# Performance work log

Measured on AMD Instinct MI355X. Metric: run time of the kernel, lower is better.

Reference implementation:

```python
import jax, jax.numpy as jnp
import numpy as np

B, D, K, A, P = 4096, 512, 128, 32, 16  # batch, theta dim, mixture comps, alpha dim, hutchinson probes


def setup_inputs() -> dict:
    key = jax.random.key(0)
    k1, k2, k3, k4 = jax.random.split(key, 4)
    thetas = jax.random.normal(k1, (B, D), dtype=jnp.float32)
    alpha = jax.random.normal(k2, (K, A), dtype=jnp.float32)
    W = jax.random.normal(k3, (A, D), dtype=jnp.float32) / jnp.sqrt(jnp.float32(A))
    v_int = jax.random.randint(k4, (P, B, D), 0, 2, dtype=jnp.int32)  # -> Rademacher via 2v-1
    return {"thetas": thetas, "alpha": alpha, "W": W, "v_int": v_int,
            "N_dataset": 100000, "K_alpha_samples": K}


def _log_density(thetas, alpha, W, N_dataset, K_alpha):
    # Tempered Gaussian mixture: mu_k = alpha_k @ W;
    # logp_b = (N/(N+1)) * (logsumexp_k -0.5||theta_b - mu_k||^2 - log K)
    mu = alpha @ W                                        # [K, D]
    # ||t - mu||^2 expanded to avoid a [B,K,D] intermediate
    sq = (jnp.sum(thetas * thetas, -1, keepdims=True)
          - 2.0 * thetas @ mu.T
          + jnp.sum(mu * mu, -1)[None, :])                # [B, K]
    temper = jnp.float32(N_dataset) / (jnp.float32(N_dataset) + 1.0)
    return temper * (jax.nn.logsumexp(-0.5 * sq, axis=1) - jnp.log(jnp.float32(K_alpha)))


def reference(thetas, alpha, W, v_int, N_dataset, K_alpha_samples):
    v = (2 * v_int - 1).astype(thetas.dtype)              # [P, B, D] Rademacher

    def logp_sum(t):
        return jnp.sum(_log_density(t, alpha, W, N_dataset, K_alpha_samples))

    score = jax.grad(logp_sum)                            # gradiente wrt thetas
    g = score(thetas)                                     # [B, D]

    # Hutchinson trace of the per-sample Hessian via forward-over-reverse HVPs,
    # batched over probes (fuses the torch per-probe autograd.grad loop).
    def hvp(vi):
        return jax.jvp(score, (thetas,), (vi,))[1]        # [B, D]

    Hv = jax.vmap(hvp)(v)                                 # [P, B, D]
    traces = jnp.mean(jnp.sum(v * Hv, axis=-1), axis=0)   # [B]

    loss = 0.5 * jnp.sum(g * g, axis=-1) + traces         # [B]
    return jnp.mean(loss)
```

## Files before the change

### kernel.cpp

```cpp
#include <hip/hip_runtime.h>
#include <hip/hip_bf16.h>
#include <stdint.h>

#define Bsz 4096
#define Dn  512
#define Kn  128
#define Pn  16
#define An  32
#define TB  16

typedef __attribute__((ext_vector_type(4))) float  floatx4;
typedef __attribute__((ext_vector_type(8))) short  shortx8;

__device__ __forceinline__ unsigned short f2bf(float x) {
    union { float f; uint32_t u; } v; v.f = x;
    uint32_t u = v.u;
    uint32_t r = (u + 0x7FFFu + ((u >> 16) & 1u)) >> 16;
    return (unsigned short)r;
}

__global__ __launch_bounds__(256) void k_mu(const float* __restrict__ alpha,
                                            const float* __restrict__ W,
                                            float* __restrict__ mu_f,
                                            unsigned short* __restrict__ mu_bf,
                                            float* __restrict__ munorm) {
    __shared__ float al[An];
    __shared__ float red[4];
    int k = blockIdx.x, t = threadIdx.x;
    if (t < An) al[t] = alpha[k * An + t];
    __syncthreads();
    int d0 = t, d1 = t + 256;
    float a0 = 0.f, a1 = 0.f;
#pragma unroll
    for (int a = 0; a < An; ++a) {
        float av = al[a];
        a0 = fmaf(av, W[a * Dn + d0], a0);
        a1 = fmaf(av, W[a * Dn + d1], a1);
    }
    mu_f[k * Dn + d0] = a0;  mu_f[k * Dn + d1] = a1;
    mu_bf[k * Dn + d0] = f2bf(a0);  mu_bf[k * Dn + d1] = f2bf(a1);
    float nrm = a0 * a0 + a1 * a1;
#pragma unroll
    for (int msk = 1; msk < 64; msk <<= 1) nrm += __shfl_xor(nrm, msk);
    if ((t & 63) == 0) red[t >> 6] = nrm;
    __syncthreads();
    if (t == 0) munorm[k] = red[0] + red[1] + red[2] + red[3];
}

__global__ __launch_bounds__(256) void k_gram(const float* __restrict__ mu_f,
                                              unsigned short* __restrict__ G_bf) {
    __shared__ float mi[Dn];
    __shared__ float hsum[128];
    int i = blockIdx.x, t = threadIdx.x;
    mi[t] = mu_f[i * Dn + t];
    mi[t + 256] = mu_f[i * Dn + t + 256];
    __syncthreads();
    int j = t >> 1, h = t & 1;
    const float* rj = mu_f + (size_t)j * Dn + h * 256;
    const float* ri = mi + h * 256;
    float acc = 0.f;
#pragma unroll 8
    for (int d = 0; d < 256; ++d) acc = fmaf(ri[d], rj[d], acc);
    if (h) hsum[j] = acc;
    __syncthreads();
    if (!h) G_bf[i * Kn + j] = f2bf(acc + hsum[j]);
}

__global__ __launch_bounds__(512, 2) void k_main(
    const float* __restrict__ thetas,
    const int* __restrict__ v_int,
    const unsigned short* __restrict__ mu_bf,
    const float* __restrict__ munorm,
    const unsigned short* __restrict__ G_bf,
    const int* __restrict__ Np,
    float* __restrict__ out)
{
    __shared__ short vt[TB][520];
    __shared__ float S_l[TB][132];
    __shared__ float w_l[TB][132];
    __shared__ short wbf[TB][136];
    __shared__ float part[8][TB][2];
    __shared__ float thn[TB];
    __shared__ float SwS[TB];

    const int tid = threadIdx.x;
    const int lane = tid & 63;
    const int wv = tid >> 6;
    const int m = lane & 15;
    const int q = lane >> 4;

    const int tileb = blockIdx.x >> 1;
    const int phalf = blockIdx.x & 1;
    const int b0 = tileb * TB;
    const int p0 = phalf * 8;

    const float Nf = (float)(*Np);
    const float temper = Nf / (Nf + 1.0f);

    const int kcol = wv * 16 + m;
    shortx8 mufrag[16];
    {
        const unsigned short* mb = mu_bf + (size_t)kcol * Dn + q * 8;
#pragma unroll
        for (int dc = 0; dc < 16; ++dc)
            mufrag[dc] = *(const shortx8*)(mb + dc * 32);
    }
    shortx8 gfrag[4];
    {
        const unsigned short* gb = G_bf + (size_t)kcol * Kn + q * 8;
#pragma unroll
        for (int kc = 0; kc < 4; ++kc)
            gfrag[kc] = *(const shortx8*)(gb + kc * 32);
    }

    const int r = tid >> 5;
    const int c0 = (tid & 31) * 16;
    const size_t PB = (size_t)Bsz * Dn;
    const int* vrow = v_int + (size_t)(b0 + r) * Dn + c0;

    int4 buf[2][4];
    {
        const int4* g = (const int4*)(vrow + (size_t)p0 * PB);
#pragma unroll
        for (int j = 0; j < 4; ++j) buf[0][j] = g[j];
    }
    {
        const float4* tg = (const float4*)(thetas + (size_t)(b0 + r) * Dn + c0);
        float tn = 0.f;
#pragma unroll
        for (int j = 0; j < 4; ++j) {
            float4 f = tg[j];
            tn += f.x * f.x + f.y * f.y + f.z * f.z + f.w * f.w;
            short4 h;
            h.x = (short)f2bf(f.x); h.y = (short)f2bf(f.y);
            h.z = (short)f2bf(f.z); h.w = (short)f2bf(f.w);
            *(short4*)&vt[r][c0 + j * 4] = h;
        }
#pragma unroll
        for (int msk = 1; msk < 32; msk <<= 1) tn += __shfl_xor(tn, msk);
        if ((tid & 31) == 0) thn[r] = tn;
    }
    __syncthreads();

    {
        floatx4 acc = {0.f, 0.f, 0.f, 0.f};
#pragma unroll
        for (int dc = 0; dc < 16; ++dc) {
            shortx8 a = *(const shortx8*)&vt[m][dc * 32 + q * 8];
            acc = __builtin_amdgcn_mfma_f32_16x16x32_bf16(a, mufrag[dc], acc, 0, 0, 0);
        }
#pragma unroll
        for (int i = 0; i < 4; ++i) S_l[q * 4 + i][kcol] = acc[i];
    }
    __syncthreads();

    {
        const int b = tid >> 5, s = tid & 31;
        float l[4];
        float mx = -3.4e38f;
        float tnb = thn[b];
#pragma unroll
        for (int j = 0; j < 4; ++j) {
            int k = s + 32 * j;
            l[j] = -0.5f * (tnb - 2.f * S_l[b][k] + munorm[k]);
            mx = fmaxf(mx, l[j]);
        }
#pragma unroll
        for (int msk = 1; msk < 32; msk <<= 1) mx = fmaxf(mx, __shfl_xor(mx, msk));
        float se = 0.f, ses = 0.f;
        float e[4];
#pragma unroll
        for (int j = 0; j < 4; ++j) {
            int k = s + 32 * j;
            e[j] = __expf(l[j] - mx);
            se += e[j];
            ses += e[j] * S_l[b][k];
        }
#pragma unroll
        for (int msk = 1; msk < 32; msk <<= 1) { se += __shfl_xor(se, msk); ses += __shfl_xor(ses, msk); }
        float inv = 1.f / se;
#pragma unroll
        for (int j = 0; j < 4; ++j) {
            int k = s + 32 * j;
            float wvv = e[j] * inv;
            w_l[b][k] = wvv;
            wbf[b][k] = (short)f2bf(wvv);
        }
        if (s == 0) SwS[b] = ses * inv;
    }
    __syncthreads();

    float lossA = 0.f;
    {
        floatx4 acc = {0.f, 0.f, 0.f, 0.f};
#pragma unroll
        for (int kc = 0; kc < 4; ++kc) {
            shortx8 a = *(const shortx8*)&wbf[m][kc * 32 + q * 8];
            acc = __builtin_amdgcn_mfma_f32_16x16x32_bf16(a, gfrag[kc], acc, 0, 0, 0);
        }
        float sg[4];
#pragma unroll
        for (int i = 0; i < 4; ++i) sg[i] = w_l[q * 4 + i][kcol] * acc[i];
#pragma unroll
        for (int msk = 1; msk < 16; msk <<= 1) {
#pragma unroll
            for (int i = 0; i < 4; ++i) sg[i] += __shfl_xor(sg[i], msk);
        }
        if (m == 0) {
#pragma unroll
            for (int i = 0; i < 4; ++i) part[wv][q * 4 + i][0] = sg[i];
        }
    }
    __syncthreads();
    if (tid < TB) {
        float wGw = 0.f;
#pragma unroll
        for (int w8 = 0; w8 < 8; ++w8) wGw += part[w8][tid][0];
        if (phalf == 0)
            lossA = 0.5f * temper * temper * (wGw - 2.f * SwS[tid] + thn[tid])
                    - temper * (float)Dn;
    }

    float tracc = 0.f;
#pragma unroll
    for (int p = 0; p < 8; ++p) {
        if (p < 7) {
            const int4* g = (const int4*)(vrow + (size_t)(p0 + p + 1) * PB);
#pragma unroll
            for (int j = 0; j < 4; ++j) buf[(p + 1) & 1][j] = g[j];
        }
#pragma unroll
        for (int j = 0; j < 4; ++j) {
            int4 w4 = buf[p & 1][j];
            short4 h;
            h.x = (short)(0x3F80 | ((1 - w4.x) << 15));
            h.y = (short)(0x3F80 | ((1 - w4.y) << 15));
            h.z = (short)(0x3F80 | ((1 - w4.z) << 15));
            h.w = (short)(0x3F80 | ((1 - w4.w) << 15));
            *(short4*)&vt[r][c0 + j * 4] = h;
        }
        __syncthreads();
        floatx4 acc = {0.f, 0.f, 0.f, 0.f};
#pragma unroll
        for (int dc = 0; dc < 16; ++dc) {
            shortx8 a = *(const shortx8*)&vt[m][dc * 32 + q * 8];
            acc = __builtin_amdgcn_mfma_f32_16x16x32_bf16(a, mufrag[dc], acc, 0, 0, 0);
        }
        float s1[4], s2[4];
#pragma unroll
        for (int i = 0; i < 4; ++i) {
            float T = acc[i];
            float wt = w_l[q * 4 + i][kcol];
            s1[i] = wt * T * T;
            s2[i] = wt * T;
        }
#pragma unroll
        for (int msk = 1; msk < 16; msk <<= 1) {
#pragma unroll
            for (int i = 0; i < 4; ++i) {
                s1[i] += __shfl_xor(s1[i], msk);
                s2[i] += __shfl_xor(s2[i], msk);
            }
        }
        if (m == 0) {
#pragma unroll
            for (int i = 0; i < 4; ++i) {
                part[wv][q * 4 + i][0] = s1[i];
                part[wv][q * 4 + i][1] = s2[i];
            }
        }
        __syncthreads();
        if (tid < TB) {
            float S1 = 0.f, S2 = 0.f;
#pragma unroll
            for (int w8 = 0; w8 < 8; ++w8) { S1 += part[w8][tid][0]; S2 += part[w8][tid][1]; }
            tracc += S1 - S2 * S2;
        }
    }

    if (tid < TB) {
        float res = temper * tracc * (1.0f / (float)Pn) + lossA;
#pragma unroll
        for (int msk = 1; msk < 16; msk <<= 1) res += __shfl_xor(res, msk);
        if (tid == 0) atomicAdd(out, res * (1.0f / (float)Bsz));
    }
}

extern "C" void kernel_launch(void* const* d_in, const int* in_sizes, int n_in,
                              void* d_out, int out_size, void* d_ws, size_t ws_size,
                              hipStream_t stream) {
    const float* thetas = (const float*)d_in[0];
    const float* alpha  = (const float*)d_in[1];
    const float* W      = (const float*)d_in[2];
    const int*   v_int  = (const int*)d_in[3];
    const int*   Np     = (const int*)d_in[4];

    char* ws = (char*)d_ws;
    float*          mu_f   = (float*)ws;
    unsigned short* mu_bf  = (unsigned short*)(ws + 262144);
    float*          munorm = (float*)(ws + 262144 + 131072);
    unsigned short* G_bf   = (unsigned short*)(ws + 262144 + 131072 + 1024);

    float* out = (float*)d_out;
    hipMemsetAsync(out, 0, sizeof(float), stream);
    k_mu  <<<dim3(Kn),  dim3(256), 0, stream>>>(alpha, W, mu_f, mu_bf, munorm);
    k_gram<<<dim3(Kn),  dim3(256), 0, stream>>>(mu_f, G_bf);
    k_main<<<dim3(512), dim3(512), 0, stream>>>(thetas, v_int, mu_bf, munorm, G_bf, Np, out);
}
```

Measured before the change: 224.5 us.

## Double-buffer probe tiles, MFMA gram kernel, fold memset, raise occupancy

The probe loop now double-buffers both the LDS probe tile and the partial-sum array, so each iteration needs one barrier instead of two and the reduction of the previous probe overlaps the next MFMA. The gram matrix is computed with bf16 MFMA from mu_bf in 8 blocks, which also removes the fp32 mu buffer. The output memset is folded into k_mu, gfrag loading is deferred to cut register pressure, and launch bounds are raised to 4 blocks per CU. The larger LDS footprint may cap the occupancy actually reached, and bf16 precision in the gram matrix changes numerics slightly.

```diff
diff --git a/kernel.cpp b/kernel.cpp
--- a/kernel.cpp
+++ b/kernel.cpp
@@ -21,12 +21,13 @@
 
 __global__ __launch_bounds__(256) void k_mu(const float* __restrict__ alpha,
                                             const float* __restrict__ W,
-                                            float* __restrict__ mu_f,
                                             unsigned short* __restrict__ mu_bf,
-                                            float* __restrict__ munorm) {
+                                            float* __restrict__ munorm,
+                                            float* __restrict__ out) {
     __shared__ float al[An];
     __shared__ float red[4];
     int k = blockIdx.x, t = threadIdx.x;
+    if (k == 0 && t == 0) *out = 0.f;
     if (t < An) al[t] = alpha[k * An + t];
     __syncthreads();
     int d0 = t, d1 = t + 256;
@@ -37,7 +38,6 @@
         a0 = fmaf(av, W[a * Dn + d0], a0);
         a1 = fmaf(av, W[a * Dn + d1], a1);
     }
-    mu_f[k * Dn + d0] = a0;  mu_f[k * Dn + d1] = a1;
     mu_bf[k * Dn + d0] = f2bf(a0);  mu_bf[k * Dn + d1] = f2bf(a1);
     float nrm = a0 * a0 + a1 * a1;
 #pragma unroll
@@ -47,26 +47,40 @@
     if (t == 0) munorm[k] = red[0] + red[1] + red[2] + red[3];
 }
 
-__global__ __launch_bounds__(256) void k_gram(const float* __restrict__ mu_f,
+__global__ __launch_bounds__(512) void k_gram(const unsigned short* __restrict__ mu_bf,
                                               unsigned short* __restrict__ G_bf) {
-    __shared__ float mi[Dn];
-    __shared__ float hsum[128];
-    int i = blockIdx.x, t = threadIdx.x;
-    mi[t] = mu_f[i * Dn + t];
-    mi[t + 256] = mu_f[i * Dn + t + 256];
-    __syncthreads();
-    int j = t >> 1, h = t & 1;
-    const float* rj = mu_f + (size_t)j * Dn + h * 256;
-    const float* ri = mi + h * 256;
-    float acc = 0.f;
-#pragma unroll 8
-    for (int d = 0; d < 256; ++d) acc = fmaf(ri[d], rj[d], acc);
-    if (h) hsum[j] = acc;
-    __syncthreads();
-    if (!h) G_bf[i * Kn + j] = f2bf(acc + hsum[j]);
-}
-
-__global__ __launch_bounds__(512, 2) void k_main(
+    __shared__ short at[TB][520];
+    const int tid = threadIdx.x;
+    const int lane = tid & 63;
+    const int wv = tid >> 6;
+    const int m = lane & 15;
+    const int q = lane >> 4;
+    const int i0 = blockIdx.x * TB;
+
+    const int r = tid >> 5, c0 = (tid & 31) * 16;
+    const int4* src = (const int4*)(mu_bf + (size_t)(i0 + r) * Dn + c0);
+    *(int4*)&at[r][c0]     = src[0];
+    *(int4*)&at[r][c0 + 8] = src[1];
+
+    const int kcol = wv * 16 + m;
+    shortx8 bfrag[16];
+    const unsigned short* mb = mu_bf + (size_t)kcol * Dn + q * 8;
+#pragma unroll
+    for (int dc = 0; dc < 16; ++dc) bfrag[dc] = *(const shortx8*)(mb + dc * 32);
+    __syncthreads();
+
+    floatx4 acc = {0.f, 0.f, 0.f, 0.f};
+#pragma unroll
+    for (int dc = 0; dc < 16; ++dc) {
+        shortx8 a = *(const shortx8*)&at[m][dc * 32 + q * 8];
+        acc = __builtin_amdgcn_mfma_f32_16x16x32_bf16(a, bfrag[dc], acc, 0, 0, 0);
+    }
+#pragma unroll
+    for (int i = 0; i < 4; ++i)
+        G_bf[(size_t)(i0 + q * 4 + i) * Kn + kcol] = f2bf(acc[i]);
+}
+
+__global__ __launch_bounds__(512, 4) void k_main(
     const float* __restrict__ thetas,
     const int* __restrict__ v_int,
     const unsigned short* __restrict__ mu_bf,
@@ -75,11 +89,11 @@
     const int* __restrict__ Np,
     float* __restrict__ out)
 {
-    __shared__ short vt[TB][520];
+    __shared__ short vt[2][TB][520];
     __shared__ float S_l[TB][132];
     __shared__ float w_l[TB][132];
     __shared__ short wbf[TB][136];
-    __shared__ float part[8][TB][2];
+    __shared__ float part[2][8][TB][2];
     __shared__ float thn[TB];
     __shared__ float SwS[TB];
 
@@ -105,24 +119,17 @@
         for (int dc = 0; dc < 16; ++dc)
             mufrag[dc] = *(const shortx8*)(mb + dc * 32);
     }
-    shortx8 gfrag[4];
-    {
-        const unsigned short* gb = G_bf + (size_t)kcol * Kn + q * 8;
-#pragma unroll
-        for (int kc = 0; kc < 4; ++kc)
-            gfrag[kc] = *(const shortx8*)(gb + kc * 32);
-    }
 
     const int r = tid >> 5;
     const int c0 = (tid & 31) * 16;
     const size_t PB = (size_t)Bsz * Dn;
     const int* vrow = v_int + (size_t)(b0 + r) * Dn + c0;
 
-    int4 buf[2][4];
+    int4 buf[4];
     {
         const int4* g = (const int4*)(vrow + (size_t)p0 * PB);
 #pragma unroll
-        for (int j = 0; j < 4; ++j) buf[0][j] = g[j];
+        for (int j = 0; j < 4; ++j) buf[j] = g[j];
     }
     {
         const float4* tg = (const float4*)(thetas + (size_t)(b0 + r) * Dn + c0);
@@ -134,7 +141,7 @@
             short4 h;
             h.x = (short)f2bf(f.x); h.y = (short)f2bf(f.y);
             h.z = (short)f2bf(f.z); h.w = (short)f2bf(f.w);
-            *(short4*)&vt[r][c0 + j * 4] = h;
+            *(short4*)&vt[0][r][c0 + j * 4] = h;
         }
 #pragma unroll
         for (int msk = 1; msk < 32; msk <<= 1) tn += __shfl_xor(tn, msk);
@@ -146,7 +153,7 @@
         floatx4 acc = {0.f, 0.f, 0.f, 0.f};
 #pragma unroll
         for (int dc = 0; dc < 16; ++dc) {
-            shortx8 a = *(const shortx8*)&vt[m][dc * 32 + q * 8];
+            shortx8 a = *(const shortx8*)&vt[0][m][dc * 32 + q * 8];
             acc = __builtin_amdgcn_mfma_f32_16x16x32_bf16(a, mufrag[dc], acc, 0, 0, 0);
         }
 #pragma unroll
@@ -190,8 +197,11 @@
     }
     __syncthreads();
 
-    float lossA = 0.f;
-    {
+    {
+        shortx8 gfrag[4];
+        const unsigned short* gb = G_bf + (size_t)kcol * Kn + q * 8;
+#pragma unroll
+        for (int kc = 0; kc < 4; ++kc) gfrag[kc] = *(const shortx8*)(gb + kc * 32);
         floatx4 acc = {0.f, 0.f, 0.f, 0.f};
 #pragma unroll
         for (int kc = 0; kc < 4; ++kc) {
@@ -208,42 +218,52 @@
         }
         if (m == 0) {
 #pragma unroll
-            for (int i = 0; i < 4; ++i) part[wv][q * 4 + i][0] = sg[i];
-        }
-    }
-    __syncthreads();
+            for (int i = 0; i < 4; ++i) part[0][wv][q * 4 + i][0] = sg[i];
+        }
+    }
+    __syncthreads();
+
+    float lossA = 0.f, tracc = 0.f;
     if (tid < TB) {
         float wGw = 0.f;
 #pragma unroll
-        for (int w8 = 0; w8 < 8; ++w8) wGw += part[w8][tid][0];
+        for (int w8 = 0; w8 < 8; ++w8) wGw += part[0][w8][tid][0];
         if (phalf == 0)
             lossA = 0.5f * temper * temper * (wGw - 2.f * SwS[tid] + thn[tid])
                     - temper * (float)Dn;
     }
 
-    float tracc = 0.f;
 #pragma unroll
     for (int p = 0; p < 8; ++p) {
+#pragma unroll
+        for (int j = 0; j < 4; ++j) {
+            int4 w4 = buf[j];
+            short4 h;
+            h.x = (short)(0x3F80 | ((w4.x ^ 1) << 15));
+            h.y = (short)(0x3F80 | ((w4.y ^ 1) << 15));
+            h.z = (short)(0x3F80 | ((w4.z ^ 1) << 15));
+            h.w = (short)(0x3F80 | ((w4.w ^ 1) << 15));
+            *(short4*)&vt[p & 1][r][c0 + j * 4] = h;
+        }
+        __syncthreads();
         if (p < 7) {
             const int4* g = (const int4*)(vrow + (size_t)(p0 + p + 1) * PB);
 #pragma unroll
-            for (int j = 0; j < 4; ++j) buf[(p + 1) & 1][j] = g[j];
-        }
-#pragma unroll
-        for (int j = 0; j < 4; ++j) {
-            int4 w4 = buf[p & 1][j];
-            short4 h;
-            h.x = (short)(0x3F80 | ((1 - w4.x) << 15));
-            h.y = (short)(0x3F80 | ((1 - w4.y) << 15));
-            h.z = (short)(0x3F80 | ((1 - w4.z) << 15));
-            h.w = (short)(0x3F80 | ((1 - w4.w) << 15));
-            *(short4*)&vt[r][c0 + j * 4] = h;
-        }
-        __syncthreads();
+            for (int j = 0; j < 4; ++j) buf[j] = g[j];
+        }
+        if (p > 0 && tid < TB) {
+            float S1 = 0.f, S2 = 0.f;
+#pragma unroll
+            for (int w8 = 0; w8 < 8; ++w8) {
+                S1 += part[(p - 1) & 1][w8][tid][0];
+                S2 += part[(p - 1) & 1][w8][tid][1];
+            }
+            tracc += S1 - S2 * S2;
+        }
         floatx4 acc = {0.f, 0.f, 0.f, 0.f};
 #pragma unroll
         for (int dc = 0; dc < 16; ++dc) {
-            shortx8 a = *(const shortx8*)&vt[m][dc * 32 + q * 8];
+            shortx8 a = *(const shortx8*)&vt[p & 1][m][dc * 32 + q * 8];
             acc = __builtin_amdgcn_mfma_f32_16x16x32_bf16(a, mufrag[dc], acc, 0, 0, 0);
         }
         float s1[4], s2[4];
@@ -265,20 +285,20 @@
         if (m == 0) {
 #pragma unroll
             for (int i = 0; i < 4; ++i) {
-                part[wv][q * 4 + i][0] = s1[i];
-                part[wv][q * 4 + i][1] = s2[i];
+                part[p & 1][wv][q * 4 + i][0] = s1[i];
+                part[p & 1][wv][q * 4 + i][1] = s2[i];
             }
         }
-        __syncthreads();
-        if (tid < TB) {
-            float S1 = 0.f, S2 = 0.f;
-#pragma unroll
-            for (int w8 = 0; w8 < 8; ++w8) { S1 += part[w8][tid][0]; S2 += part[w8][tid][1]; }
-            tracc += S1 - S2 * S2;
-        }
-    }
-
+    }
+    __syncthreads();
     if (tid < TB) {
+        float S1 = 0.f, S2 = 0.f;
+#pragma unroll
+        for (int w8 = 0; w8 < 8; ++w8) {
+            S1 += part[1][w8][tid][0];
+            S2 += part[1][w8][tid][1];
+        }
+        tracc += S1 - S2 * S2;
         float res = temper * tracc * (1.0f / (float)Pn) + lossA;
 #pragma unroll
         for (int msk = 1; msk < 16; msk <<= 1) res += __shfl_xor(res, msk);
@@ -296,14 +316,12 @@
     const int*   Np     = (const int*)d_in[4];
 
     char* ws = (char*)d_ws;
-    float*          mu_f   = (float*)ws;
-    unsigned short* mu_bf  = (unsigned short*)(ws + 262144);
-    float*          munorm = (float*)(ws + 262144 + 131072);
-    unsigned short* G_bf   = (unsigned short*)(ws + 262144 + 131072 + 1024);
+    unsigned short* mu_bf  = (unsigned short*)ws;
+    float*          munorm = (float*)(ws + 131072);
+    unsigned short* G_bf   = (unsigned short*)(ws + 131072 + 1024);
 
     float* out = (float*)d_out;
-    hipMemsetAsync(out, 0, sizeof(float), stream);
-    k_mu  <<<dim3(Kn),  dim3(256), 0, stream>>>(alpha, W, mu_f, mu_bf, munorm);
-    k_gram<<<dim3(Kn),  dim3(256), 0, stream>>>(mu_f, G_bf);
+    k_mu  <<<dim3(Kn), dim3(256), 0, stream>>>(alpha, W, mu_bf, munorm, out);
+    k_gram<<<dim3(8),  dim3(512), 0, stream>>>(mu_bf, G_bf);
     k_main<<<dim3(512), dim3(512), 0, stream>>>(thetas, v_int, mu_bf, munorm, G_bf, Np, out);
 }
```

After: 217.9 us. -2.9%, faster.
